# Kernel optimization log

Hardware: AMD Instinct MI355X
Metric: run time of the kernel (lower is better)

The kernel has to match this reference:

```python
import jax, jax.numpy as jnp
import numpy as np
import math

EMBED_DIM = 1024
NUM_HEADS = 16
HEAD_DIM = EMBED_DIM // NUM_HEADS
BATCH = 2
SEQ = 2048
GATE_EPS = 1e-4


def setup_inputs() -> dict:
    key = jax.random.key(0)
    ks = jax.random.split(key, 6)
    scale_e = 1.0 / math.sqrt(EMBED_DIM)
    scale_h = 1.0 / math.sqrt(HEAD_DIM)
    return {
        "hidden_states": jax.random.normal(ks[0], (BATCH, SEQ, EMBED_DIM), dtype=jnp.float32),
        "attention_mask": jnp.zeros((BATCH, 1, 1, SEQ), dtype=jnp.float32),
        "W_q": jax.random.normal(ks[1], (NUM_HEADS, EMBED_DIM, HEAD_DIM), dtype=jnp.float32) * scale_e,
        "W_k": jax.random.normal(ks[2], (NUM_HEADS, EMBED_DIM, HEAD_DIM), dtype=jnp.float32) * scale_e,
        "W_v": jax.random.normal(ks[3], (NUM_HEADS, EMBED_DIM, HEAD_DIM), dtype=jnp.float32) * scale_e,
        "W_o": jax.random.normal(ks[4], (NUM_HEADS, HEAD_DIM, EMBED_DIM), dtype=jnp.float32) * scale_h,
        "gate": jnp.ones((NUM_HEADS,), dtype=jnp.float32),
    }


def reference(hidden_states, attention_mask, W_q, W_k, W_v, W_o, gate):
    # Effective gate: heads with gate < 1e-4 are skipped (contribute zero).
    eff_gate = jnp.where(gate >= GATE_EPS, gate, 0.0)  # [H]

    # Batched per-head projections: x [B,S,E], W [H,E,D] -> [B,H,S,D]
    q = jnp.einsum("bse,hed->bhsd", hidden_states, W_q)
    k = jnp.einsum("bse,hed->bhsd", hidden_states, W_k)
    v = jnp.einsum("bse,hed->bhsd", hidden_states, W_v)

    scores = jnp.einsum("bhsd,bhtd->bhst", q, k) / math.sqrt(HEAD_DIM)
    scores = scores + attention_mask  # [B,1,1,S] broadcasts over heads/queries
    probs = jax.nn.softmax(scores, axis=-1)

    context = jnp.einsum("bhst,bhtd->bhsd", probs, v)
    head_out = jnp.einsum("bhsd,hde->bhse", context, W_o)

    out = jnp.einsum("h,bhse->bse", eff_gate, head_out)

    # Final rescale: divide by max(1, active_gates / num_heads) when any head active.
    active = jnp.sum((gate > GATE_EPS).astype(jnp.float32))
    denom = jnp.maximum(1.0, active / NUM_HEADS)
    out = jnp.where(active > 0, out / denom, out)
    return out
```

## Files before the change

kernel.cpp:

```cpp
#include <hip/hip_runtime.h>
#include <hip/hip_bf16.h>

typedef short bf16x4 __attribute__((ext_vector_type(4)));
typedef short bf16x8 __attribute__((ext_vector_type(8)));
typedef float f32x4  __attribute__((ext_vector_type(4)));

#define LOG2E 1.4426950408889634f
#define QSCALE (0.125f * LOG2E)

__device__ __forceinline__ short f2bf(float x) {
  union { __hip_bfloat16 h; short s; } u;
  u.h = __float2bfloat16(x);
  return u.s;
}

__device__ __forceinline__ float fast_exp2(float x) {
#if __has_builtin(__builtin_amdgcn_exp2f)
  return __builtin_amdgcn_exp2f(x);
#else
  return exp2f(x);
#endif
}

__device__ __forceinline__ void load16_lds(const void* g, void* l) {
#if __has_builtin(__builtin_amdgcn_global_load_lds)
  __builtin_amdgcn_global_load_lds(
      (const __attribute__((address_space(1))) unsigned int*)g,
      (__attribute__((address_space(3))) unsigned int*)l, 16, 0, 0);
#else
  const int lane = threadIdx.x & 63;
  *(bf16x8*)((char*)l + lane * 16) = *(const bf16x8*)((const char*)g + lane * 16);
#endif
}

__global__ __launch_bounds__(256)
void cvt_x_kernel(const float* __restrict__ in, short* __restrict__ out, int n4) {
  for (int i = blockIdx.x * blockDim.x + threadIdx.x; i < n4; i += gridDim.x * blockDim.x) {
    const float4 v = ((const float4*)in)[i];
    bf16x4 o;
    o[0] = f2bf(v.x); o[1] = f2bf(v.y); o[2] = f2bf(v.z); o[3] = f2bf(v.w);
    ((bf16x4*)out)[i] = o;
  }
}

__global__ __launch_bounds__(256)
void trans_all_kernel(const float* __restrict__ Wq, const float* __restrict__ Wk,
                      const float* __restrict__ Wv, const float* __restrict__ Wo,
                      short* __restrict__ Wt3, short* __restrict__ Wot) {
  __shared__ float t[32][33];
  const int f = blockIdx.x;
  const float* in;
  short* out;
  int R, C, r0, c0;
  if (f < 3072) {
    const int which = f >> 10;
    const int rem = f & 1023;
    const int z = rem >> 6;
    const int xy = rem & 63;
    in = (which == 0 ? Wq : which == 1 ? Wk : Wv) + (size_t)z * 65536;
    out = Wt3 + (size_t)which * 1048576 + (size_t)z * 65536;
    R = 1024; C = 64; r0 = (xy >> 1) * 32; c0 = (xy & 1) * 32;
  } else {
    const int rem = f - 3072;
    in = Wo; out = Wot;
    R = 1024; C = 1024; r0 = (rem >> 5) * 32; c0 = (rem & 31) * 32;
  }
  const int tr = threadIdx.x >> 5, tc = threadIdx.x & 31;
#pragma unroll
  for (int p = 0; p < 4; ++p)
    t[tr + p * 8][tc] = in[(size_t)(r0 + tr + p * 8) * C + c0 + tc];
  __syncthreads();
#pragma unroll
  for (int p = 0; p < 4; ++p)
    out[(size_t)(c0 + tr + p * 8) * R + r0 + tc] = f2bf(t[tc][tr + p * 8]);
}

__global__ __launch_bounds__(256)
void gemm_qkv_kernel(const short* __restrict__ A, const short* __restrict__ Bt,
                     short* __restrict__ Qb, short* __restrict__ Kb,
                     short* __restrict__ Vt) {
  __shared__ short Al[128 * 32];
  __shared__ short Bl[128 * 32];
  const int tid = threadIdx.x;
  const int w = tid >> 6, lane = tid & 63;
  const int lq = lane & 15, lg = lane >> 4;
  const int m0 = blockIdx.x * 128, n0 = blockIdx.y * 128;
  const int which = n0 >> 10;
  const int wr = (w >> 1) * 64, wc = (w & 1) * 64;

  f32x4 acc[4][4] = {};
  const int grow = lane >> 2;
  const int gcol = (lane & 3) * 8;

  for (int k0 = 0; k0 < 1024; k0 += 32) {
#pragma unroll
    for (int c = 0; c < 2; ++c) {
      const int chunk = (w << 1) | c;
      const int row = chunk * 16 + grow;
      load16_lds(A + (size_t)(m0 + row) * 1024 + k0 + gcol, &Al[chunk * 512]);
      load16_lds(Bt + (size_t)(n0 + row) * 1024 + k0 + gcol, &Bl[chunk * 512]);
    }
    __syncthreads();
    bf16x8 af[4], bfr[4];
#pragma unroll
    for (int i = 0; i < 4; ++i)
      af[i] = *(const bf16x8*)&Al[(wr + i * 16 + lq) * 32 + lg * 8];
#pragma unroll
    for (int j = 0; j < 4; ++j)
      bfr[j] = *(const bf16x8*)&Bl[(wc + j * 16 + lq) * 32 + lg * 8];
    if (which < 2) {
#pragma unroll
      for (int i = 0; i < 4; ++i)
#pragma unroll
        for (int j = 0; j < 4; ++j)
          acc[i][j] = __builtin_amdgcn_mfma_f32_16x16x32_bf16(bfr[j], af[i], acc[i][j], 0, 0, 0);
    } else {
#pragma unroll
      for (int i = 0; i < 4; ++i)
#pragma unroll
        for (int j = 0; j < 4; ++j)
          acc[i][j] = __builtin_amdgcn_mfma_f32_16x16x32_bf16(af[i], bfr[j], acc[i][j], 0, 0, 0);
    }
    __syncthreads();
  }

  if (which < 2) {
    short* Out = which ? Kb : Qb;
    const float sc = which ? 1.f : QSCALE;
    const int m = m0 + wr + lq;
#pragma unroll
    for (int i = 0; i < 4; ++i) {
      const int mm = m + i * 16;
      const int b = mm >> 11, s = mm & 2047;
#pragma unroll
      for (int j = 0; j < 4; ++j) {
        const int nn = (n0 + wc + j * 16 + lg * 4) & 1023;
        const int h = nn >> 6, d = nn & 63;
        bf16x4 o;
#pragma unroll
        for (int r = 0; r < 4; ++r) o[r] = f2bf(acc[i][j][r] * sc);
        *(bf16x4*)&Out[(size_t)((b * 16 + h) * 2048 + s) * 64 + d] = o;
      }
    }
  } else {
#pragma unroll
    for (int i = 0; i < 4; ++i) {
      const int mb = m0 + wr + i * 16 + lg * 4;
      const int b = mb >> 11, s = mb & 2047;
#pragma unroll
      for (int j = 0; j < 4; ++j) {
        const int nn = (n0 + wc + j * 16 + lq) & 1023;
        const int h = nn >> 6, d = nn & 63;
        bf16x4 o;
#pragma unroll
        for (int r = 0; r < 4; ++r) o[r] = f2bf(acc[i][j][r]);
        *(bf16x4*)&Vt[(size_t)((b * 16 + h) * 64 + d) * 2048 + s] = o;
      }
    }
  }
}

__global__ __launch_bounds__(256)
void gemm_out_kernel(const short* __restrict__ A, const short* __restrict__ Bt,
                     float* __restrict__ Out) {
  __shared__ short Al[64 * 32];
  __shared__ short Bl[128 * 32];
  const int tid = threadIdx.x;
  const int w = tid >> 6, lane = tid & 63;
  const int lq = lane & 15, lg = lane >> 4;
  const int m0 = blockIdx.x * 64, n0 = blockIdx.y * 128;
  const int wr = (w >> 1) * 32, wc = (w & 1) * 64;

  f32x4 acc[2][4] = {};
  const int grow = lane >> 2;
  const int gcol = (lane & 3) * 8;

  for (int k0 = 0; k0 < 1024; k0 += 32) {
    {
      const int arow = w * 16 + grow;
      load16_lds(A + (size_t)(m0 + arow) * 1024 + k0 + gcol, &Al[w * 512]);
#pragma unroll
      for (int c = 0; c < 2; ++c) {
        const int chunk = (w << 1) | c;
        const int row = chunk * 16 + grow;
        load16_lds(Bt + (size_t)(n0 + row) * 1024 + k0 + gcol, &Bl[chunk * 512]);
      }
    }
    __syncthreads();
    bf16x8 af[2], bfr[4];
#pragma unroll
    for (int i = 0; i < 2; ++i)
      af[i] = *(const bf16x8*)&Al[(wr + i * 16 + lq) * 32 + lg * 8];
#pragma unroll
    for (int j = 0; j < 4; ++j)
      bfr[j] = *(const bf16x8*)&Bl[(wc + j * 16 + lq) * 32 + lg * 8];
#pragma unroll
    for (int i = 0; i < 2; ++i)
#pragma unroll
      for (int j = 0; j < 4; ++j)
        acc[i][j] = __builtin_amdgcn_mfma_f32_16x16x32_bf16(af[i], bfr[j], acc[i][j], 0, 0, 0);
    __syncthreads();
  }

#pragma unroll
  for (int i = 0; i < 2; ++i)
#pragma unroll
    for (int r = 0; r < 4; ++r) {
      const int m = m0 + wr + i * 16 + lg * 4 + r;
      float* orow = Out + (size_t)m * 1024 + n0 + wc;
#pragma unroll
      for (int j = 0; j < 4; ++j) orow[j * 16 + lq] = acc[i][j][r];
    }
}

__global__ __launch_bounds__(256, 2)
void attn_kernel(const short* __restrict__ Qb, const short* __restrict__ Kb,
                 const short* __restrict__ Vt, const float* __restrict__ mask,
                 const float* __restrict__ gate, short* __restrict__ ctx) {
  __shared__ __align__(16) char lds[66560];

  const int tid = threadIdx.x;
  const int w = tid >> 6, lane = tid & 63;
  const int lq = lane & 15, lg = lane >> 4;
  const int l = blockIdx.x;
  const int bh = (l & 7) * 4 + (l >> 8);
  const int q0 = ((l >> 3) & 31) * 64;
  const int b = bh >> 4, h = bh & 15;
  const size_t bhoff = (size_t)bh * 2048 * 64;

  const float g = gate[h];
  const float eff = (g >= 1e-4f) ? g : 0.f;
  int active = 0;
#pragma unroll
  for (int j = 0; j < 16; ++j) active += (gate[j] > 1e-4f) ? 1 : 0;
  const float gsc = eff / fmaxf(1.f, (float)active / 16.f);

  bf16x8 qf[4][2];
#pragma unroll
  for (int qt = 0; qt < 4; ++qt) {
    const short* qp = Qb + bhoff + (size_t)(q0 + qt * 16 + lq) * 64 + lg * 8;
    qf[qt][0] = *(const bf16x8*)qp;
    qf[qt][1] = *(const bf16x8*)(qp + 32);
  }

  const int koffs = (lane >> 3) * 128 + (((lane & 7) * 16) ^ ((lane >> 3) << 4));
  const int vrowc = lane >> 4;
  const int vs_e = ((lane & 15) * 16) ^ (vrowc << 4);
  const int vs_o = ((lane & 15) * 16) ^ ((vrowc + 4) << 4);
  const char* KbB = (const char*)(Kb + bhoff);
  const char* VtB = (const char*)(Vt + bhoff);

  const int sw = (lq & 7) << 4;
  const int kcol0 = (lg * 16) ^ sw, kcol1 = (64 + lg * 16) ^ sw;
  const int vcol0 = (w * 64 + lg * 8) ^ sw, vcol1 = (w * 64 + 32 + lg * 8) ^ sw;
  const float* maskp = mask + b * 2048;

  f32x4 acc[4][4] = {};
  f32x4 lacc[4] = {};

#define STAGE(T, P)                                                              \
  {                                                                              \
    char* kd = lds + (P)*16384 + w * 4096;                                       \
    const char* ks = KbB + (size_t)((T)*128 + w * 32) * 128 + koffs;             \
    char* vd = lds + 32768 + (P)*16384 + w * 4096;                               \
    const char* vsb = VtB + (size_t)(w * 16 + vrowc) * 4096 + (T)*256;           \
    load16_lds(ks, kd);                                                          \
    load16_lds(ks + 1024, kd + 1024);                                            \
    load16_lds(ks + 2048, kd + 2048);                                            \
    load16_lds(ks + 3072, kd + 3072);                                            \
    load16_lds(vsb + vs_e, vd);                                                  \
    load16_lds(vsb + 16384 + vs_o, vd + 1024);                                   \
    load16_lds(vsb + 32768 + vs_e, vd + 2048);                                   \
    load16_lds(vsb + 49152 + vs_o, vd + 3072);                                   \
  }

  STAGE(0, 0);
  __syncthreads();

  for (int t = 0; t < 16; ++t) {
    const int cur = t & 1;
    const f32x4 mk0 = *(const f32x4*)(maskp + t * 128 + w * 32 + lg * 4);
    const f32x4 mk1 = *(const f32x4*)(maskp + t * 128 + w * 32 + 16 + lg * 4);
    if (t < 15) STAGE(t + 1, cur ^ 1);

    const char* Kc = lds + cur * 16384 + (w * 32 + lq) * 128;
    f32x4 s[2][4];
#pragma unroll
    for (int kt = 0; kt < 2; ++kt) {
      const bf16x8 ka0 = *(const bf16x8*)(Kc + kt * 2048 + kcol0);
      const bf16x8 ka1 = *(const bf16x8*)(Kc + kt * 2048 + kcol1);
#pragma unroll
      for (int qt = 0; qt < 4; ++qt) {
        f32x4 ts = {};
        ts = __builtin_amdgcn_mfma_f32_16x16x32_bf16(ka0, qf[qt][0], ts, 0, 0, 0);
        ts = __builtin_amdgcn_mfma_f32_16x16x32_bf16(ka1, qf[qt][1], ts, 0, 0, 0);
        s[kt][qt] = ts;
      }
    }

    bf16x4 pf[2][4];
#pragma unroll
    for (int kt = 0; kt < 2; ++kt) {
      const f32x4 mkv = kt ? mk1 : mk0;
#pragma unroll
      for (int qt = 0; qt < 4; ++qt) {
        const float p0 = fast_exp2(fmaf(mkv[0], LOG2E, s[kt][qt][0]));
        const float p1 = fast_exp2(fmaf(mkv[1], LOG2E, s[kt][qt][1]));
        const float p2 = fast_exp2(fmaf(mkv[2], LOG2E, s[kt][qt][2]));
        const float p3 = fast_exp2(fmaf(mkv[3], LOG2E, s[kt][qt][3]));
        pf[kt][qt][0] = f2bf(p0); pf[kt][qt][1] = f2bf(p1);
        pf[kt][qt][2] = f2bf(p2); pf[kt][qt][3] = f2bf(p3);
        const f32x4 pv = {p0, p1, p2, p3};
        lacc[qt] += pv;
      }
    }

    bf16x8 pb[4];
#pragma unroll
    for (int qt = 0; qt < 4; ++qt)
      pb[qt] = __builtin_shufflevector(pf[0][qt], pf[1][qt], 0, 1, 2, 3, 4, 5, 6, 7);
#pragma unroll
    for (int dt = 0; dt < 4; ++dt) {
      const char* Vrow = lds + 32768 + cur * 16384 + (dt * 16 + lq) * 256;
      const bf16x4 v0 = *(const bf16x4*)(Vrow + vcol0);
      const bf16x4 v1 = *(const bf16x4*)(Vrow + vcol1);
      const bf16x8 av = __builtin_shufflevector(v0, v1, 0, 1, 2, 3, 4, 5, 6, 7);
#pragma unroll
      for (int qt = 0; qt < 4; ++qt)
        acc[dt][qt] = __builtin_amdgcn_mfma_f32_16x16x32_bf16(av, pb[qt], acc[dt][qt], 0, 0, 0);
    }

    __syncthreads();
  }
#undef STAGE

#pragma unroll
  for (int dt = 0; dt < 4; ++dt)
#pragma unroll
    for (int qt = 0; qt < 4; ++qt)
      *(f32x4*)(lds + w * 16384 + (qt * 16 + lq) * 256 + ((dt * 64 + lg * 16) ^ sw)) =
          acc[dt][qt];

  float* Lb = (float*)(lds + 65536);
#pragma unroll
  for (int qt = 0; qt < 4; ++qt) {
    float lt = (lacc[qt][0] + lacc[qt][1]) + (lacc[qt][2] + lacc[qt][3]);
    lt += __shfl_xor(lt, 16);
    lt += __shfl_xor(lt, 32);
    if (lg == 0) Lb[w * 64 + qt * 16 + lq] = lt;
  }
  __syncthreads();

  const float lsum = Lb[w * 16 + lq] + Lb[64 + w * 16 + lq] +
                     Lb[128 + w * 16 + lq] + Lb[192 + w * 16 + lq];
  const float osc = gsc / lsum;
  const int qabs = q0 + w * 16 + lq;
#pragma unroll
  for (int dt = 0; dt < 4; ++dt) {
    const int dby = (dt * 64 + lg * 16) ^ sw;
    f32x4 o = *(const f32x4*)(lds + (w * 16 + lq) * 256 + dby);
    o += *(const f32x4*)(lds + 16384 + (w * 16 + lq) * 256 + dby);
    o += *(const f32x4*)(lds + 32768 + (w * 16 + lq) * 256 + dby);
    o += *(const f32x4*)(lds + 49152 + (w * 16 + lq) * 256 + dby);
    bf16x4 ob;
#pragma unroll
    for (int r = 0; r < 4; ++r) ob[r] = f2bf(o[r] * osc);
    *(bf16x4*)&ctx[(size_t)(b * 2048 + qabs) * 1024 + h * 64 + dt * 16 + lg * 4] = ob;
  }
}

extern "C" void kernel_launch(void* const* d_in, const int* in_sizes, int n_in,
                              void* d_out, int out_size, void* d_ws, size_t ws_size,
                              hipStream_t stream) {
  (void)in_sizes; (void)n_in; (void)out_size; (void)ws_size;
  const float* x    = (const float*)d_in[0];
  const float* mask = (const float*)d_in[1];
  const float* Wq   = (const float*)d_in[2];
  const float* Wk   = (const float*)d_in[3];
  const float* Wv   = (const float*)d_in[4];
  const float* Wo   = (const float*)d_in[5];
  const float* gate = (const float*)d_in[6];
  float* out = (float*)d_out;

  char* ws = (char*)d_ws;
  const size_t MB = 1024 * 1024;
  short* Xb  = (short*)(ws + 256);
  short* Wt3 = (short*)(ws + 256 + 8 * MB);
  short* Wot = (short*)(ws + 256 + 14 * MB);
  short* Qb  = (short*)(ws + 256 + 16 * MB);
  short* Kb  = (short*)(ws + 256 + 24 * MB);
  short* Vt  = (short*)(ws + 256 + 32 * MB);
  short* ctx = (short*)(ws + 256 + 40 * MB);

  cvt_x_kernel<<<2048, 256, 0, stream>>>(x, Xb, 4194304 / 4);
  trans_all_kernel<<<4096, 256, 0, stream>>>(Wq, Wk, Wv, Wo, Wt3, Wot);
  gemm_qkv_kernel<<<dim3(32, 24), 256, 0, stream>>>(Xb, Wt3, Qb, Kb, Vt);
  attn_kernel<<<1024, 256, 0, stream>>>(Qb, Kb, Vt, mask, gate, ctx);
  gemm_out_kernel<<<dim3(64, 8), 256, 0, stream>>>(ctx, Wot, out);
}
```

Baseline: 206.3 us.

## Single-buffer attention LDS for higher occupancy and merge prep kernels

The attention kernel drops K/V double buffering and shrinks its shared memory to about 33 KB. Its launch bound rises to 4 blocks per CU, and the cross-wave output reduction is split into two halves so it fits the smaller buffer. Separately, the x-to-bf16 conversion and the weight transposes are merged into one prep kernel to save a launch. The trade is that global-to-LDS loads are no longer overlapped with MFMA work inside a block, so the design relies on extra resident blocks to hide latency, and the halved reduction adds barriers.

```diff
diff --git a/kernel.cpp b/kernel.cpp
--- a/kernel.cpp
+++ b/kernel.cpp
@@ -34,21 +34,24 @@
 }
 
 __global__ __launch_bounds__(256)
-void cvt_x_kernel(const float* __restrict__ in, short* __restrict__ out, int n4) {
-  for (int i = blockIdx.x * blockDim.x + threadIdx.x; i < n4; i += gridDim.x * blockDim.x) {
-    const float4 v = ((const float4*)in)[i];
-    bf16x4 o;
-    o[0] = f2bf(v.x); o[1] = f2bf(v.y); o[2] = f2bf(v.z); o[3] = f2bf(v.w);
-    ((bf16x4*)out)[i] = o;
-  }
-}
-
-__global__ __launch_bounds__(256)
-void trans_all_kernel(const float* __restrict__ Wq, const float* __restrict__ Wk,
-                      const float* __restrict__ Wv, const float* __restrict__ Wo,
-                      short* __restrict__ Wt3, short* __restrict__ Wot) {
+void prep_kernel(const float* __restrict__ x, const float* __restrict__ Wq,
+                 const float* __restrict__ Wk, const float* __restrict__ Wv,
+                 const float* __restrict__ Wo, short* __restrict__ Xb,
+                 short* __restrict__ Wt3, short* __restrict__ Wot) {
+  const int f = blockIdx.x;
+  if (f >= 4096) {
+    const int base = (f - 4096) * 1024 + threadIdx.x;
+#pragma unroll
+    for (int p = 0; p < 4; ++p) {
+      const int i = base + p * 256;
+      const float4 v = ((const float4*)x)[i];
+      bf16x4 o;
+      o[0] = f2bf(v.x); o[1] = f2bf(v.y); o[2] = f2bf(v.z); o[3] = f2bf(v.w);
+      ((bf16x4*)Xb)[i] = o;
+    }
+    return;
+  }
   __shared__ float t[32][33];
-  const int f = blockIdx.x;
   const float* in;
   short* out;
   int R, C, r0, c0;
@@ -213,11 +216,11 @@
     }
 }
 
-__global__ __launch_bounds__(256, 2)
+__global__ __launch_bounds__(256, 4)
 void attn_kernel(const short* __restrict__ Qb, const short* __restrict__ Kb,
                  const short* __restrict__ Vt, const float* __restrict__ mask,
                  const float* __restrict__ gate, short* __restrict__ ctx) {
-  __shared__ __align__(16) char lds[66560];
+  __shared__ __align__(16) char lds[33792];
 
   const int tid = threadIdx.x;
   const int w = tid >> 6, lane = tid & 63;
@@ -258,32 +261,26 @@
   f32x4 acc[4][4] = {};
   f32x4 lacc[4] = {};
 
-#define STAGE(T, P)                                                              \
-  {                                                                              \
-    char* kd = lds + (P)*16384 + w * 4096;                                       \
-    const char* ks = KbB + (size_t)((T)*128 + w * 32) * 128 + koffs;             \
-    char* vd = lds + 32768 + (P)*16384 + w * 4096;                               \
-    const char* vsb = VtB + (size_t)(w * 16 + vrowc) * 4096 + (T)*256;           \
-    load16_lds(ks, kd);                                                          \
-    load16_lds(ks + 1024, kd + 1024);                                            \
-    load16_lds(ks + 2048, kd + 2048);                                            \
-    load16_lds(ks + 3072, kd + 3072);                                            \
-    load16_lds(vsb + vs_e, vd);                                                  \
-    load16_lds(vsb + 16384 + vs_o, vd + 1024);                                   \
-    load16_lds(vsb + 32768 + vs_e, vd + 2048);                                   \
-    load16_lds(vsb + 49152 + vs_o, vd + 3072);                                   \
-  }
-
-  STAGE(0, 0);
-  __syncthreads();
-
   for (int t = 0; t < 16; ++t) {
-    const int cur = t & 1;
     const f32x4 mk0 = *(const f32x4*)(maskp + t * 128 + w * 32 + lg * 4);
     const f32x4 mk1 = *(const f32x4*)(maskp + t * 128 + w * 32 + 16 + lg * 4);
-    if (t < 15) STAGE(t + 1, cur ^ 1);
-
-    const char* Kc = lds + cur * 16384 + (w * 32 + lq) * 128;
+    {
+      char* kd = lds + w * 4096;
+      const char* ks = KbB + (size_t)(t * 128 + w * 32) * 128 + koffs;
+      char* vd = lds + 16384 + w * 4096;
+      const char* vsb = VtB + (size_t)(w * 16 + vrowc) * 4096 + t * 256;
+      load16_lds(ks, kd);
+      load16_lds(ks + 1024, kd + 1024);
+      load16_lds(ks + 2048, kd + 2048);
+      load16_lds(ks + 3072, kd + 3072);
+      load16_lds(vsb + vs_e, vd);
+      load16_lds(vsb + 16384 + vs_o, vd + 1024);
+      load16_lds(vsb + 32768 + vs_e, vd + 2048);
+      load16_lds(vsb + 49152 + vs_o, vd + 3072);
+    }
+    __syncthreads();
+
+    const char* Kc = lds + (w * 32 + lq) * 128;
     f32x4 s[2][4];
 #pragma unroll
     for (int kt = 0; kt < 2; ++kt) {
@@ -321,7 +318,7 @@
       pb[qt] = __builtin_shufflevector(pf[0][qt], pf[1][qt], 0, 1, 2, 3, 4, 5, 6, 7);
 #pragma unroll
     for (int dt = 0; dt < 4; ++dt) {
-      const char* Vrow = lds + 32768 + cur * 16384 + (dt * 16 + lq) * 256;
+      const char* Vrow = lds + 16384 + (dt * 16 + lq) * 256;
       const bf16x4 v0 = *(const bf16x4*)(Vrow + vcol0);
       const bf16x4 v1 = *(const bf16x4*)(Vrow + vcol1);
       const bf16x8 av = __builtin_shufflevector(v0, v1, 0, 1, 2, 3, 4, 5, 6, 7);
@@ -332,16 +329,8 @@
 
     __syncthreads();
   }
-#undef STAGE
-
-#pragma unroll
-  for (int dt = 0; dt < 4; ++dt)
-#pragma unroll
-    for (int qt = 0; qt < 4; ++qt)
-      *(f32x4*)(lds + w * 16384 + (qt * 16 + lq) * 256 + ((dt * 64 + lg * 16) ^ sw)) =
-          acc[dt][qt];
-
-  float* Lb = (float*)(lds + 65536);
+
+  float* Lb = (float*)(lds + 32768);
 #pragma unroll
   for (int qt = 0; qt < 4; ++qt) {
     float lt = (lacc[qt][0] + lacc[qt][1]) + (lacc[qt][2] + lacc[qt][3]);
@@ -349,23 +338,54 @@
     lt += __shfl_xor(lt, 32);
     if (lg == 0) Lb[w * 64 + qt * 16 + lq] = lt;
   }
+
+#pragma unroll
+  for (int dtl = 0; dtl < 2; ++dtl)
+#pragma unroll
+    for (int qt = 0; qt < 4; ++qt)
+      *(f32x4*)(lds + w * 8192 + (qt * 16 + lq) * 128 + ((dtl * 64 + lg * 16) ^ sw)) =
+          acc[dtl][qt];
   __syncthreads();
 
   const float lsum = Lb[w * 16 + lq] + Lb[64 + w * 16 + lq] +
                      Lb[128 + w * 16 + lq] + Lb[192 + w * 16 + lq];
   const float osc = gsc / lsum;
   const int qabs = q0 + w * 16 + lq;
-#pragma unroll
-  for (int dt = 0; dt < 4; ++dt) {
-    const int dby = (dt * 64 + lg * 16) ^ sw;
-    f32x4 o = *(const f32x4*)(lds + (w * 16 + lq) * 256 + dby);
-    o += *(const f32x4*)(lds + 16384 + (w * 16 + lq) * 256 + dby);
-    o += *(const f32x4*)(lds + 32768 + (w * 16 + lq) * 256 + dby);
-    o += *(const f32x4*)(lds + 49152 + (w * 16 + lq) * 256 + dby);
+  short* ctxp = ctx + (size_t)(b * 2048 + qabs) * 1024 + h * 64;
+
+#pragma unroll
+  for (int dtl = 0; dtl < 2; ++dtl) {
+    const int dby = (dtl * 64 + lg * 16) ^ sw;
+    f32x4 o = *(const f32x4*)(lds + (w * 16 + lq) * 128 + dby);
+    o += *(const f32x4*)(lds + 8192 + (w * 16 + lq) * 128 + dby);
+    o += *(const f32x4*)(lds + 16384 + (w * 16 + lq) * 128 + dby);
+    o += *(const f32x4*)(lds + 24576 + (w * 16 + lq) * 128 + dby);
     bf16x4 ob;
 #pragma unroll
     for (int r = 0; r < 4; ++r) ob[r] = f2bf(o[r] * osc);
-    *(bf16x4*)&ctx[(size_t)(b * 2048 + qabs) * 1024 + h * 64 + dt * 16 + lg * 4] = ob;
+    *(bf16x4*)&ctxp[dtl * 16 + lg * 4] = ob;
+  }
+  __syncthreads();
+
+#pragma unroll
+  for (int dtl = 0; dtl < 2; ++dtl)
+#pragma unroll
+    for (int qt = 0; qt < 4; ++qt)
+      *(f32x4*)(lds + w * 8192 + (qt * 16 + lq) * 128 + ((dtl * 64 + lg * 16) ^ sw)) =
+          acc[2 + dtl][qt];
+  __syncthreads();
+
+#pragma unroll
+  for (int dtl = 0; dtl < 2; ++dtl) {
+    const int dby = (dtl * 64 + lg * 16) ^ sw;
+    f32x4 o = *(const f32x4*)(lds + (w * 16 + lq) * 128 + dby);
+    o += *(const f32x4*)(lds + 8192 + (w * 16 + lq) * 128 + dby);
+    o += *(const f32x4*)(lds + 16384 + (w * 16 + lq) * 128 + dby);
+    o += *(const f32x4*)(lds + 24576 + (w * 16 + lq) * 128 + dby);
+    bf16x4 ob;
+#pragma unroll
+    for (int r = 0; r < 4; ++r) ob[r] = f2bf(o[r] * osc);
+    *(bf16x4*)&ctxp[32 + dtl * 16 + lg * 4] = ob;
   }
 }
 
@@ -392,8 +412,7 @@
   short* Vt  = (short*)(ws + 256 + 32 * MB);
   short* ctx = (short*)(ws + 256 + 40 * MB);
 
-  cvt_x_kernel<<<2048, 256, 0, stream>>>(x, Xb, 4194304 / 4);
-  trans_all_kernel<<<4096, 256, 0, stream>>>(Wq, Wk, Wv, Wo, Wt3, Wot);
+  prep_kernel<<<5120, 256, 0, stream>>>(x, Wq, Wk, Wv, Wo, Xb, Wt3, Wot);
   gemm_qkv_kernel<<<dim3(32, 24), 256, 0, stream>>>(Xb, Wt3, Qb, Kb, Vt);
   attn_kernel<<<1024, 256, 0, stream>>>(Qb, Kb, Vt, mask, gate, ctx);
   gemm_out_kernel<<<dim3(64, 8), 256, 0, stream>>>(ctx, Wot, out);
```

Measured after the change: 394.0 us. 1.91x slower.
